# Kernel tuning notes

Hardware: AMD Instinct MI355X
Metric: run time of the kernel (lower is better)

Reference implementation:

```python
import jax, jax.numpy as jnp
import numpy as np

EPS = 0.5


def setup_inputs() -> dict:
    key = jax.random.key(0)
    k_x, k_e, k_w1, k_b1, k_w2, k_b2 = jax.random.split(key, 6)
    N, E = 100000, 600000
    D_IN, D_HID, D_OUT = 128, 256, 128
    x = jax.random.normal(k_x, (N, D_IN), dtype=jnp.float32)
    edge_index = jax.random.randint(k_e, (2, E), 0, N, dtype=jnp.int64)
    # nn.Linear params: weight [out, in], bias [out]; kaiming-uniform-ish init
    lim1 = 1.0 / np.sqrt(D_IN)
    W1 = jax.random.uniform(k_w1, (D_HID, D_IN), minval=-lim1, maxval=lim1, dtype=jnp.float32)
    b1 = jax.random.uniform(k_b1, (D_HID,), minval=-lim1, maxval=lim1, dtype=jnp.float32)
    lim2 = 1.0 / np.sqrt(D_HID)
    W2 = jax.random.uniform(k_w2, (D_OUT, D_HID), minval=-lim2, maxval=lim2, dtype=jnp.float32)
    b2 = jax.random.uniform(k_b2, (D_OUT,), minval=-lim2, maxval=lim2, dtype=jnp.float32)
    return {"x": x, "edge_index": edge_index, "W1": W1, "b1": b1, "W2": W2, "b2": b2}


def reference(x, edge_index, W1, b1, W2, b2):
    # gather both endpoint features per edge and sum: [E, D_IN]
    s = x[edge_index[0]] + x[edge_index[1]]
    # 2-layer MLP: Linear -> ReLU -> Linear
    h = jax.nn.relu(s @ W1.T + b1)          # [E, D_HID]
    edge_attr = h @ W2.T + b2               # [E, D_OUT]
    return EPS * edge_attr
```

## Files before the change

kernel.cpp:

```cpp
#include <hip/hip_runtime.h>
#include <hip/hip_bf16.h>

#define EDGES 600000
#define DIN 128
#define DHID 256
#define DOUT 128
#define NNODES 100000

#define NCHUNK 37500
#define NBLK 256
#define THREADS 768
#define STRIDE 3072

#define W2_OFF 65536
#define B1_OFF 131072
#define B2_OFF 132096
#define LDS_BYTES 132608

#define XB_OFF_SHORTS 65536
#define WS_BYTES_NEEDED (131072ull + (unsigned long long)NNODES * DIN * 2ull)

typedef __attribute__((ext_vector_type(4))) float floatx4;
typedef __attribute__((ext_vector_type(4))) short shortx4;
typedef __attribute__((ext_vector_type(8))) short shortx8;

__device__ inline unsigned short f2bf_rne(float f) {
    union { float f; unsigned u; } v; v.f = f;
    unsigned r = v.u + 0x7FFFu + ((v.u >> 16) & 1u);
    return (unsigned short)(r >> 16);
}

__global__ __launch_bounds__(256) void prep_kernel(
        const float* __restrict__ W1, const float* __restrict__ W2,
        unsigned short* __restrict__ ws) {
    int j = blockIdx.x * 256 + threadIdx.x;
    if (j < 4096) {
        int lane = j & 63, fs = j >> 6;
        int ks = fs & 3, t = fs >> 2;
        int hid = t * 16 + (lane & 15), q = lane >> 4;
        const float* src = W1 + hid * DIN + ks * 32 + q * 8;
        shortx8 v;
        #pragma unroll
        for (int i = 0; i < 8; ++i) v[i] = (short)f2bf_rne(src[i]);
        *((shortx8*)ws + j) = v;
    } else if (j < 12288) {
        int j2 = j - 4096;
        int lane = j2 & 63, fs = j2 >> 6;
        int ot = fs & 7, t = fs >> 3;
        int o = ot * 16 + (lane & 15), q = lane >> 4;
        const float* src = W2 + o * DHID + t * 16 + q * 4;
        shortx4 v;
        #pragma unroll
        for (int i = 0; i < 4; ++i) v[i] = (short)f2bf_rne(src[i]);
        *((shortx4*)(ws + 32768) + j2) = v;
    }
}

__global__ __launch_bounds__(256) void prep_x(
        const float* __restrict__ x, unsigned short* __restrict__ xb) {
    const int total = NNODES * DIN / 4;
    for (int i = blockIdx.x * 256 + threadIdx.x; i < total; i += gridDim.x * 256) {
        float4 v = ((const float4*)x)[i];
        shortx4 o;
        o[0] = (short)f2bf_rne(v.x); o[1] = (short)f2bf_rne(v.y);
        o[2] = (short)f2bf_rne(v.z); o[3] = (short)f2bf_rne(v.w);
        *((shortx4*)xb + i) = o;
    }
}

template <bool BFX>
__global__ __launch_bounds__(THREADS, 3) void gin_kernel(
        const float* __restrict__ x, const unsigned short* __restrict__ xb,
        const int* __restrict__ ei,
        const float* __restrict__ b1, const float* __restrict__ b2,
        const unsigned short* __restrict__ wsw,
        float* __restrict__ out) {
    extern __shared__ char smem[];
    const int tid = threadIdx.x;
    const int lane = tid & 63, q = lane >> 4, col = lane & 15;

    const int gw = blockIdx.x * 12 + (tid >> 6);
    int ch = gw;

    float4  rawf[BFX ? 1 : 16];
    shortx8 rawb[BFX ? 8 : 1];

    auto gather = [&](int na, int nb) {
        if constexpr (BFX) {
            const shortx8* pa = (const shortx8*)xb + (size_t)na * 16 + q;
            const shortx8* pb = (const shortx8*)xb + (size_t)nb * 16 + q;
            #pragma unroll
            for (int ks = 0; ks < 4; ++ks) {
                rawb[ks*2+0] = pa[ks*4];
                rawb[ks*2+1] = pb[ks*4];
            }
        } else {
            const float* pa = x + (size_t)na * DIN + q * 8;
            const float* pb = x + (size_t)nb * DIN + q * 8;
            #pragma unroll
            for (int ks = 0; ks < 4; ++ks) {
                rawf[ks*4+0] = *(const float4*)(pa + ks*32);
                rawf[ks*4+1] = *(const float4*)(pa + ks*32 + 4);
                rawf[ks*4+2] = *(const float4*)(pb + ks*32);
                rawf[ks*4+3] = *(const float4*)(pb + ks*32 + 4);
            }
        }
    };

    const int e0 = ch * 16 + col;
    const int na0 = ei[e0];
    const int nb0 = ei[EDGES + e0];

    {
        const float4* gsrc = (const float4*)wsw;
        for (int idx = tid; idx < 8192; idx += THREADS) {
            float4 v = gsrc[idx];
            *(float4*)(smem + (size_t)idx * 16) = v;
        }
        if (tid < 384) {
            float v = (tid < 256) ? b1[tid] : b2[tid - 256];
            *(float*)(smem + B1_OFF + tid * 4) = v;
        }
    }

    gather(na0, nb0);

    int naN, nbN;
    {
        const int e1 = (ch + STRIDE) * 16 + col;
        naN = ei[e1];
        nbN = ei[EDGES + e1];
    }
    __syncthreads();

    const shortx8* w1l = (const shortx8*)smem + lane;
    const shortx4* w2l = (const shortx4*)(smem + W2_OFF) + lane;
    const floatx4* b1l = (const floatx4*)(smem + B1_OFF) + q;
    const floatx4* b2l = (const floatx4*)(smem + B2_OFF) + q;

    for (;;) {
        shortx8 sfrag[4];
        if constexpr (BFX) {
            #pragma unroll
            for (int ks = 0; ks < 4; ++ks) {
                union { shortx8 s8; __hip_bfloat162 h[4]; } A, B, S;
                A.s8 = rawb[ks*2]; B.s8 = rawb[ks*2+1];
                #pragma unroll
                for (int j = 0; j < 4; ++j) {
                    float2 fa = __bfloat1622float2(A.h[j]);
                    float2 fb = __bfloat1622float2(B.h[j]);
                    S.h[j] = __float22bfloat162_rn(make_float2(fa.x + fb.x, fa.y + fb.y));
                }
                sfrag[ks] = S.s8;
            }
        } else {
            #pragma unroll
            for (int ks = 0; ks < 4; ++ks) {
                float4 u0 = rawf[ks*4+0], u1 = rawf[ks*4+1];
                float4 v0 = rawf[ks*4+2], v1 = rawf[ks*4+3];
                union { shortx8 s8; __hip_bfloat162 b[4]; } pk;
                pk.b[0] = __float22bfloat162_rn(make_float2(u0.x+v0.x, u0.y+v0.y));
                pk.b[1] = __float22bfloat162_rn(make_float2(u0.z+v0.z, u0.w+v0.w));
                pk.b[2] = __float22bfloat162_rn(make_float2(u1.x+v1.x, u1.y+v1.y));
                pk.b[3] = __float22bfloat162_rn(make_float2(u1.z+v1.z, u1.w+v1.w));
                sfrag[ks] = pk.s8;
            }
        }

        const int chN = ch + STRIDE;
        const bool haveN = (chN < NCHUNK);
        if (haveN) {
            gather(naN, nbN);
            const int ch2 = chN + STRIDE;
            if (ch2 < NCHUNK) {
                const int e2 = ch2 * 16 + col;
                naN = ei[e2];
                nbN = ei[EDGES + e2];
            }
        }

        floatx4 acc2[8];
        #pragma unroll
        for (int ot = 0; ot < 8; ++ot) acc2[ot] = b2l[ot*4];

        #pragma unroll 1
        for (int t = 0; t < 16; ++t) {
            shortx8 a1[4];
            #pragma unroll
            for (int ks = 0; ks < 4; ++ks) a1[ks] = w1l[(t*4+ks)*64];
            floatx4 acc1 = b1l[t*4];
            #pragma unroll
            for (int ks = 0; ks < 4; ++ks)
                acc1 = __builtin_amdgcn_mfma_f32_16x16x32_bf16(a1[ks], sfrag[ks], acc1, 0, 0, 0);
            union { shortx4 s4; __hip_bfloat162 b[2]; } pk;
            pk.b[0] = __float22bfloat162_rn(make_float2(fmaxf(acc1[0], 0.f), fmaxf(acc1[1], 0.f)));
            pk.b[1] = __float22bfloat162_rn(make_float2(fmaxf(acc1[2], 0.f), fmaxf(acc1[3], 0.f)));
            const shortx4 hf = pk.s4;
            #pragma unroll
            for (int ot = 0; ot < 8; ++ot) {
                shortx4 wb = w2l[(t*8+ot)*64];
                acc2[ot] = __builtin_amdgcn_mfma_f32_16x16x16bf16_1k(wb, hf, acc2[ot], 0, 0, 0);
            }
        }

        {
            float* op = out + (size_t)(ch * 16 + col) * DOUT + q * 4;
            #pragma unroll
            for (int ot = 0; ot < 8; ++ot) {
                floatx4 v = acc2[ot] * 0.5f;
                *(floatx4*)(op + ot * 16) = v;
            }
        }

        if (!haveN) break;
        ch = chN;
    }
}

extern "C" void kernel_launch(void* const* d_in, const int* in_sizes, int n_in,
                              void* d_out, int out_size, void* d_ws, size_t ws_size,
                              hipStream_t stream) {
    const float* x  = (const float*)d_in[0];
    const int*   ei = (const int*)d_in[1];
    const float* W1 = (const float*)d_in[2];
    const float* b1 = (const float*)d_in[3];
    const float* W2 = (const float*)d_in[4];
    const float* b2 = (const float*)d_in[5];
    unsigned short* ws = (unsigned short*)d_ws;

    static bool attr_done = false;
    if (!attr_done) {
        (void)hipFuncSetAttribute((const void*)gin_kernel<true>,
                                  hipFuncAttributeMaxDynamicSharedMemorySize,
                                  LDS_BYTES);
        (void)hipFuncSetAttribute((const void*)gin_kernel<false>,
                                  hipFuncAttributeMaxDynamicSharedMemorySize,
                                  LDS_BYTES);
        attr_done = true;
    }

    prep_kernel<<<48, 256, 0, stream>>>(W1, W2, ws);
    if (ws_size >= WS_BYTES_NEEDED) {
        unsigned short* xb = ws + XB_OFF_SHORTS;
        prep_x<<<2048, 256, 0, stream>>>(x, xb);
        gin_kernel<true><<<NBLK, THREADS, LDS_BYTES, stream>>>(
            x, xb, ei, b1, b2, ws, (float*)d_out);
    } else {
        gin_kernel<false><<<NBLK, THREADS, LDS_BYTES, stream>>>(
            x, nullptr, ei, b1, b2, ws, (float*)d_out);
    }
}
```

Baseline: 435.8 us.

## Process 32 edges per wave to reuse LDS weight fragments across two tiles

Each wave now handles two 16-edge groups per chunk, so every W1/W2 fragment read from LDS feeds two MFMAs. W2 is repacked into 8-element fragments covering two output tiles, which halves the number of W2 LDS loads. Block size drops from 768 to 512 threads with occupancy hint 2 to make room for the doubled register footprint. The fp32 gather path now converts to bf16 at load time. The risks are higher register pressure and fewer waves available to hide gather latency.

```diff
diff --git a/kernel.cpp b/kernel.cpp
--- a/kernel.cpp
+++ b/kernel.cpp
@@ -7,10 +7,11 @@
 #define DOUT 128
 #define NNODES 100000
 
-#define NCHUNK 37500
+#define EPB 32
+#define NCHUNK 18750
 #define NBLK 256
-#define THREADS 768
-#define STRIDE 3072
+#define THREADS 512
+#define STRIDE 2048
 
 #define W2_OFF 65536
 #define B1_OFF 131072
@@ -43,16 +44,20 @@
         #pragma unroll
         for (int i = 0; i < 8; ++i) v[i] = (short)f2bf_rne(src[i]);
         *((shortx8*)ws + j) = v;
-    } else if (j < 12288) {
+    } else if (j < 8192) {
         int j2 = j - 4096;
         int lane = j2 & 63, fs = j2 >> 6;
-        int ot = fs & 7, t = fs >> 3;
-        int o = ot * 16 + (lane & 15), q = lane >> 4;
-        const float* src = W2 + o * DHID + t * 16 + q * 4;
-        shortx4 v;
-        #pragma unroll
-        for (int i = 0; i < 4; ++i) v[i] = (short)f2bf_rne(src[i]);
-        *((shortx4*)(ws + 32768) + j2) = v;
+        int op = fs & 3, t = fs >> 2;
+        int m = lane & 15, q = lane >> 4;
+        const float* lo = W2 + (size_t)(op * 32 + m) * DHID + t * 16 + q * 4;
+        const float* hi = W2 + (size_t)(op * 32 + 16 + m) * DHID + t * 16 + q * 4;
+        shortx8 v;
+        #pragma unroll
+        for (int i = 0; i < 4; ++i) {
+            v[i]     = (short)f2bf_rne(lo[i]);
+            v[4 + i] = (short)f2bf_rne(hi[i]);
+        }
+        *((shortx8*)(ws + 32768) + j2) = v;
     }
 }
 
@@ -69,7 +74,7 @@
 }
 
 template <bool BFX>
-__global__ __launch_bounds__(THREADS, 3) void gin_kernel(
+__global__ __launch_bounds__(THREADS, 2) void gin_kernel(
         const float* __restrict__ x, const unsigned short* __restrict__ xb,
         const int* __restrict__ ei,
         const float* __restrict__ b1, const float* __restrict__ b2,
@@ -79,37 +84,58 @@
     const int tid = threadIdx.x;
     const int lane = tid & 63, q = lane >> 4, col = lane & 15;
 
-    const int gw = blockIdx.x * 12 + (tid >> 6);
+    const int gw = blockIdx.x * 8 + (tid >> 6);
     int ch = gw;
 
-    float4  rawf[BFX ? 1 : 16];
-    shortx8 rawb[BFX ? 8 : 1];
-
-    auto gather = [&](int na, int nb) {
-        if constexpr (BFX) {
-            const shortx8* pa = (const shortx8*)xb + (size_t)na * 16 + q;
-            const shortx8* pb = (const shortx8*)xb + (size_t)nb * 16 + q;
-            #pragma unroll
-            for (int ks = 0; ks < 4; ++ks) {
-                rawb[ks*2+0] = pa[ks*4];
-                rawb[ks*2+1] = pb[ks*4];
-            }
-        } else {
-            const float* pa = x + (size_t)na * DIN + q * 8;
-            const float* pb = x + (size_t)nb * DIN + q * 8;
-            #pragma unroll
-            for (int ks = 0; ks < 4; ++ks) {
-                rawf[ks*4+0] = *(const float4*)(pa + ks*32);
-                rawf[ks*4+1] = *(const float4*)(pa + ks*32 + 4);
-                rawf[ks*4+2] = *(const float4*)(pb + ks*32);
-                rawf[ks*4+3] = *(const float4*)(pb + ks*32 + 4);
+    shortx8 rawb[2][8];
+
+    auto gather = [&](const int* na, const int* nb) {
+        #pragma unroll
+        for (int g = 0; g < 2; ++g) {
+            if constexpr (BFX) {
+                const shortx8* pa = (const shortx8*)xb + (size_t)na[g] * 16 + q;
+                const shortx8* pb = (const shortx8*)xb + (size_t)nb[g] * 16 + q;
+                #pragma unroll
+                for (int ks = 0; ks < 4; ++ks) {
+                    rawb[g][ks*2+0] = pa[ks*4];
+                    rawb[g][ks*2+1] = pb[ks*4];
+                }
+            } else {
+                const float* pa = x + (size_t)na[g] * DIN + q * 8;
+                const float* pb = x + (size_t)nb[g] * DIN + q * 8;
+                #pragma unroll
+                for (int ks = 0; ks < 4; ++ks) {
+                    float4 u0 = *(const float4*)(pa + ks*32);
+                    float4 u1 = *(const float4*)(pa + ks*32 + 4);
+                    float4 v0 = *(const float4*)(pb + ks*32);
+                    float4 v1 = *(const float4*)(pb + ks*32 + 4);
+                    shortx8 sa, sb;
+                    sa[0]=(short)f2bf_rne(u0.x); sa[1]=(short)f2bf_rne(u0.y);
+                    sa[2]=(short)f2bf_rne(u0.z); sa[3]=(short)f2bf_rne(u0.w);
+                    sa[4]=(short)f2bf_rne(u1.x); sa[5]=(short)f2bf_rne(u1.y);
+                    sa[6]=(short)f2bf_rne(u1.z); sa[7]=(short)f2bf_rne(u1.w);
+                    sb[0]=(short)f2bf_rne(v0.x); sb[1]=(short)f2bf_rne(v0.y);
+                    sb[2]=(short)f2bf_rne(v0.z); sb[3]=(short)f2bf_rne(v0.w);
+                    sb[4]=(short)f2bf_rne(v1.x); sb[5]=(short)f2bf_rne(v1.y);
+                    sb[6]=(short)f2bf_rne(v1.z); sb[7]=(short)f2bf_rne(v1.w);
+                    rawb[g][ks*2+0] = sa;
+                    rawb[g][ks*2+1] = sb;
+                }
             }
         }
     };
 
-    const int e0 = ch * 16 + col;
-    const int na0 = ei[e0];
-    const int nb0 = ei[EDGES + e0];
+    auto load_ei = [&](int c, int* na, int* nb) {
+        #pragma unroll
+        for (int g = 0; g < 2; ++g) {
+            const int e = c * EPB + g * 16 + col;
+            na[g] = ei[e];
+            nb[g] = ei[EDGES + e];
+        }
+    };
+
+    int na0[2], nb0[2], naN[2], nbN[2];
+    load_ei(ch, na0, nb0);
 
     {
         const float4* gsrc = (const float4*)wsw;
@@ -124,46 +150,29 @@
     }
 
     gather(na0, nb0);
-
-    int naN, nbN;
-    {
-        const int e1 = (ch + STRIDE) * 16 + col;
-        naN = ei[e1];
-        nbN = ei[EDGES + e1];
-    }
+    load_ei(ch + STRIDE < NCHUNK ? ch + STRIDE : ch, naN, nbN);
     __syncthreads();
 
     const shortx8* w1l = (const shortx8*)smem + lane;
-    const shortx4* w2l = (const shortx4*)(smem + W2_OFF) + lane;
+    const shortx8* w2l = (const shortx8*)(smem + W2_OFF) + lane;
     const floatx4* b1l = (const floatx4*)(smem + B1_OFF) + q;
     const floatx4* b2l = (const floatx4*)(smem + B2_OFF) + q;
 
     for (;;) {
-        shortx8 sfrag[4];
-        if constexpr (BFX) {
+        shortx8 sfrag[2][4];
+        #pragma unroll
+        for (int g = 0; g < 2; ++g) {
             #pragma unroll
             for (int ks = 0; ks < 4; ++ks) {
                 union { shortx8 s8; __hip_bfloat162 h[4]; } A, B, S;
-                A.s8 = rawb[ks*2]; B.s8 = rawb[ks*2+1];
+                A.s8 = rawb[g][ks*2]; B.s8 = rawb[g][ks*2+1];
                 #pragma unroll
                 for (int j = 0; j < 4; ++j) {
                     float2 fa = __bfloat1622float2(A.h[j]);
                     float2 fb = __bfloat1622float2(B.h[j]);
                     S.h[j] = __float22bfloat162_rn(make_float2(fa.x + fb.x, fa.y + fb.y));
                 }
-                sfrag[ks] = S.s8;
-            }
-        } else {
-            #pragma unroll
-            for (int ks = 0; ks < 4; ++ks) {
-                float4 u0 = rawf[ks*4+0], u1 = rawf[ks*4+1];
-                float4 v0 = rawf[ks*4+2], v1 = rawf[ks*4+3];
-                union { shortx8 s8; __hip_bfloat162 b[4]; } pk;
-                pk.b[0] = __float22bfloat162_rn(make_float2(u0.x+v0.x, u0.y+v0.y));
-                pk.b[1] = __float22bfloat162_rn(make_float2(u0.z+v0.z, u0.w+v0.w));
-                pk.b[2] = __float22bfloat162_rn(make_float2(u1.x+v1.x, u1.y+v1.y));
-                pk.b[3] = __float22bfloat162_rn(make_float2(u1.z+v1.z, u1.w+v1.w));
-                sfrag[ks] = pk.s8;
+                sfrag[g][ks] = S.s8;
             }
         }
 
@@ -172,43 +181,56 @@
         if (haveN) {
             gather(naN, nbN);
             const int ch2 = chN + STRIDE;
-            if (ch2 < NCHUNK) {
-                const int e2 = ch2 * 16 + col;
-                naN = ei[e2];
-                nbN = ei[EDGES + e2];
-            }
-        }
-
-        floatx4 acc2[8];
-        #pragma unroll
-        for (int ot = 0; ot < 8; ++ot) acc2[ot] = b2l[ot*4];
+            if (ch2 < NCHUNK) load_ei(ch2, naN, nbN);
+        }
+
+        floatx4 acc2[2][8];
+        #pragma unroll
+        for (int ot = 0; ot < 8; ++ot) {
+            floatx4 bv = b2l[ot*4];
+            acc2[0][ot] = bv;
+            acc2[1][ot] = bv;
+        }
 
         #pragma unroll 1
         for (int t = 0; t < 16; ++t) {
             shortx8 a1[4];
             #pragma unroll
             for (int ks = 0; ks < 4; ++ks) a1[ks] = w1l[(t*4+ks)*64];
-            floatx4 acc1 = b1l[t*4];
-            #pragma unroll
-            for (int ks = 0; ks < 4; ++ks)
-                acc1 = __builtin_amdgcn_mfma_f32_16x16x32_bf16(a1[ks], sfrag[ks], acc1, 0, 0, 0);
-            union { shortx4 s4; __hip_bfloat162 b[2]; } pk;
-            pk.b[0] = __float22bfloat162_rn(make_float2(fmaxf(acc1[0], 0.f), fmaxf(acc1[1], 0.f)));
-            pk.b[1] = __float22bfloat162_rn(make_float2(fmaxf(acc1[2], 0.f), fmaxf(acc1[3], 0.f)));
-            const shortx4 hf = pk.s4;
+            const floatx4 bv1 = b1l[t*4];
+            floatx4 acc1[2];
+            acc1[0] = bv1; acc1[1] = bv1;
+            #pragma unroll
+            for (int ks = 0; ks < 4; ++ks) {
+                acc1[0] = __builtin_amdgcn_mfma_f32_16x16x32_bf16(a1[ks], sfrag[0][ks], acc1[0], 0, 0, 0);
+                acc1[1] = __builtin_amdgcn_mfma_f32_16x16x32_bf16(a1[ks], sfrag[1][ks], acc1[1], 0, 0, 0);
+            }
+            shortx4 hf[2];
+            #pragma unroll
+            for (int g = 0; g < 2; ++g) {
+                union { shortx4 s4; __hip_bfloat162 b[2]; } pk;
+                pk.b[0] = __float22bfloat162_rn(make_float2(fmaxf(acc1[g][0], 0.f), fmaxf(acc1[g][1], 0.f)));
+                pk.b[1] = __float22bfloat162_rn(make_float2(fmaxf(acc1[g][2], 0.f), fmaxf(acc1[g][3], 0.f)));
+                hf[g] = pk.s4;
+            }
+            #pragma unroll
+            for (int op = 0; op < 4; ++op) {
+                union { shortx8 s8; shortx4 s4[2]; } w;
+                w.s8 = w2l[(t*4+op)*64];
+                acc2[0][op*2+0] = __builtin_amdgcn_mfma_f32_16x16x16bf16_1k(w.s4[0], hf[0], acc2[0][op*2+0], 0, 0, 0);
+                acc2[1][op*2+0] = __builtin_amdgcn_mfma_f32_16x16x16bf16_1k(w.s4[0], hf[1], acc2[1][op*2+0], 0, 0, 0);
+                acc2[0][op*2+1] = __builtin_amdgcn_mfma_f32_16x16x16bf16_1k(w.s4[1], hf[0], acc2[0][op*2+1], 0, 0, 0);
+                acc2[1][op*2+1] = __builtin_amdgcn_mfma_f32_16x16x16bf16_1k(w.s4[1], hf[1], acc2[1][op*2+1], 0, 0, 0);
+            }
+        }
+
+        #pragma unroll
+        for (int g = 0; g < 2; ++g) {
+            float* op_ = out + (size_t)(ch * EPB + g * 16 + col) * DOUT + q * 4;
             #pragma unroll
             for (int ot = 0; ot < 8; ++ot) {
-                shortx4 wb = w2l[(t*8+ot)*64];
-                acc2[ot] = __builtin_amdgcn_mfma_f32_16x16x16bf16_1k(wb, hf, acc2[ot], 0, 0, 0);
-            }
-        }
-
-        {
-            float* op = out + (size_t)(ch * 16 + col) * DOUT + q * 4;
-            #pragma unroll
-            for (int ot = 0; ot < 8; ++ot) {
-                floatx4 v = acc2[ot] * 0.5f;
-                *(floatx4*)(op + ot * 16) = v;
+                floatx4 v = acc2[g][ot] * 0.5f;
+                *(floatx4*)(op_ + ot * 16) = v;
             }
         }
 
```

Measured after the change: 435.9 us. Within noise of the previous version (+0.0%).
